# Kernel tuning notes

Hardware: AMD Instinct MI355X
Metric: run time of the kernel (lower is better)

Reference implementation:

```python
import jax, jax.numpy as jnp
import numpy as np

EPS = 1e-6
TAU = 0.07


def setup_inputs() -> dict:
    key = jax.random.key(0)
    kx, ky = jax.random.split(key)
    B, D = 4096, 1024
    x = jax.random.normal(kx, (B, D), dtype=jnp.float32)
    y = jax.random.normal(ky, (B, D), dtype=jnp.float32)
    return {"x": x, "y": y}


def reference(x, y):
    B = x.shape[0]
    # torch CosineSimilarity: dot / (max(||x||, eps) * max(||y||, eps))
    xn = x / jnp.maximum(jnp.linalg.norm(x, axis=-1, keepdims=True), EPS)
    yn = y / jnp.maximum(jnp.linalg.norm(y, axis=-1, keepdims=True), EPS)
    S = jnp.einsum('id,jd->ij', xn, yn)          # [B, B] cosine sims, S[i,j]=cos(x_i,y_j)
    E = jnp.exp(S / TAU)                          # bounded: |S|<=1 so exp <= e^{1/0.07}
    diag = jnp.diagonal(E)
    # original: sum_j (exp + eps) + eps  ->  sum_j exp + B*eps + eps
    extra = B * EPS + EPS
    row_denom = jnp.sum(E, axis=1) + extra        # x->y direction (loop 1)
    col_denom = jnp.sum(E, axis=0) + extra        # y->x direction (loop 2)
    coef = -1.0 / (2.0 * B)
    loss = coef * (jnp.sum(jnp.log(diag / row_denom)) + jnp.sum(jnp.log(diag / col_denom)))
    return loss
```

## Files before the change

### kernel.cpp

```cpp
#include <hip/hip_runtime.h>
#include <hip/hip_bf16.h>

#define NB 4096
#define DK 1024
#define EPSF 1e-6f
#define QSCALE 16.0f

typedef __attribute__((ext_vector_type(8))) int   i32x8_t;
typedef __attribute__((ext_vector_type(4))) int   i32x4_t;
typedef __attribute__((ext_vector_type(4))) float f32x4_t;


__global__ __launch_bounds__(256) void normalize_rows(
    const float* __restrict__ x, const float* __restrict__ y,
    unsigned char* __restrict__ xq, unsigned char* __restrict__ yq,
    float* __restrict__ sdiag, float* __restrict__ zerobuf)
{
    const int t = threadIdx.x;
    const int gid = blockIdx.x * 256 + t;
    if (gid < 2 * NB) zerobuf[gid] = 0.f;

    const int wave = t >> 6;
    const int lane = t & 63;
    const int row  = blockIdx.x * 4 + wave;

    const float4* xr = reinterpret_cast<const float4*>(x + (size_t)row * DK);
    const float4* yr = reinterpret_cast<const float4*>(y + (size_t)row * DK);

    float4 xv[4], yv[4];
    float ssx = 0.f, ssy = 0.f, sxy = 0.f;
    #pragma unroll
    for (int jj = 0; jj < 4; ++jj) {
        xv[jj] = xr[lane * 4 + jj];
        yv[jj] = yr[lane * 4 + jj];
        ssx += xv[jj].x*xv[jj].x + xv[jj].y*xv[jj].y + xv[jj].z*xv[jj].z + xv[jj].w*xv[jj].w;
        ssy += yv[jj].x*yv[jj].x + yv[jj].y*yv[jj].y + yv[jj].z*yv[jj].z + yv[jj].w*yv[jj].w;
        sxy += xv[jj].x*yv[jj].x + xv[jj].y*yv[jj].y + xv[jj].z*yv[jj].z + xv[jj].w*yv[jj].w;
    }
    #pragma unroll
    for (int off = 1; off < 64; off <<= 1) {
        ssx += __shfl_xor(ssx, off, 64);
        ssy += __shfl_xor(ssy, off, 64);
        sxy += __shfl_xor(sxy, off, 64);
    }
    const float invx = 1.0f / fmaxf(sqrtf(ssx), EPSF);
    const float invy = 1.0f / fmaxf(sqrtf(ssy), EPSF);
    const float sx = invx * QSCALE;
    const float sy = invy * QSCALE;

    i32x4_t xb, yb;
    #pragma unroll
    for (int jj = 0; jj < 4; ++jj) {
        int px = __builtin_amdgcn_cvt_pk_fp8_f32(xv[jj].x * sx, xv[jj].y * sx, 0, false);
        px     = __builtin_amdgcn_cvt_pk_fp8_f32(xv[jj].z * sx, xv[jj].w * sx, px, true);
        int py = __builtin_amdgcn_cvt_pk_fp8_f32(yv[jj].x * sy, yv[jj].y * sy, 0, false);
        py     = __builtin_amdgcn_cvt_pk_fp8_f32(yv[jj].z * sy, yv[jj].w * sy, py, true);
        xb[jj] = px;
        yb[jj] = py;
    }

    const int p = row >> 4, r = row & 15;
    const unsigned off = (unsigned)(p * 32 + (lane >> 3) * 4 + ((lane >> 1) & 3)) * 512
                       + r * 32 + (lane & 1) * 16;
    *reinterpret_cast<i32x4_t*>(xq + off) = xb;
    *reinterpret_cast<i32x4_t*>(yq + off) = yb;

    if (lane == 0) sdiag[row] = sxy * invx * invy;
}

__device__ __forceinline__ i32x8_t ldfrag(const unsigned char* p) {
    const i32x4_t lo = *reinterpret_cast<const i32x4_t*>(p);
    const i32x4_t hi = *reinterpret_cast<const i32x4_t*>(p + 16);
    i32x8_t r;
    r[0] = lo[0]; r[1] = lo[1]; r[2] = lo[2]; r[3] = lo[3];
    r[4] = hi[0]; r[5] = hi[1]; r[6] = hi[2]; r[7] = hi[3];
    return r;
}

__global__ __launch_bounds__(256) void gemm_exp_sums(
    const unsigned char* __restrict__ xq, const unsigned char* __restrict__ yq,
    float* __restrict__ rowsum, float* __restrict__ colsum)
{
    const int t    = threadIdx.x;
    const int lane = t & 63;
    const int wave = t >> 6;
    const int q    = lane >> 4;
    const int l15  = lane & 15;

    const int R0 = blockIdx.y * 128;
    const int C0 = blockIdx.x * 128;
    const int wRow = (wave >> 1) * 64;
    const int wCol = (wave & 1) * 64;

    f32x4_t acc[4][4];
    #pragma unroll
    for (int i = 0; i < 4; i++)
        #pragma unroll
        for (int j = 0; j < 4; j++)
            acc[i][j] = (f32x4_t){0.f, 0.f, 0.f, 0.f};

    const unsigned char* Abase =
        xq + (size_t)(((R0 + wRow) >> 4) * 32 + q) * 512 + l15 * 32;
    const unsigned char* Bbase =
        yq + (size_t)(((C0 + wCol) >> 4) * 32 + q) * 512 + l15 * 32;

    const int kb0 = (2 * wave + (blockIdx.x & 1)) & 7;

    #pragma unroll 1
    for (int s = 0; s < 8; ++s) {
        const int kb = (kb0 + s) & 7;
        const unsigned char* Ak = Abase + kb * 2048;
        const unsigned char* Bk = Bbase + kb * 2048;

        i32x8_t bfr[4], afr[4];
        #pragma unroll
        for (int nt = 0; nt < 4; ++nt) bfr[nt] = ldfrag(Bk + nt * 16384);
        #pragma unroll
        for (int mt = 0; mt < 4; ++mt) afr[mt] = ldfrag(Ak + mt * 16384);

        #pragma unroll
        for (int mt = 0; mt < 4; ++mt)
            #pragma unroll
            for (int nt = 0; nt < 4; ++nt)
                acc[mt][nt] = __builtin_amdgcn_mfma_scale_f32_16x16x128_f8f6f4(
                    afr[mt], bfr[nt], acc[mt][nt],
                    0, 0,
                    0, 0x7F7F7F7F,
                    0, 0x7F7F7F7F);
    }

    const float kScale = (float)(1.0 / (256.0 * 0.07 * 0.6931471805599453));
    float csum[4] = {0.f, 0.f, 0.f, 0.f};
    #pragma unroll
    for (int mt = 0; mt < 4; ++mt) {
        float rsum[4] = {0.f, 0.f, 0.f, 0.f};
        #pragma unroll
        for (int nt = 0; nt < 4; ++nt) {
            #pragma unroll
            for (int r = 0; r < 4; ++r) {
                const float e = exp2f(acc[mt][nt][r] * kScale);
                rsum[r]  += e;
                csum[nt] += e;
            }
        }
        #pragma unroll
        for (int r = 0; r < 4; ++r) {
            float v = rsum[r];
            v += __shfl_xor(v, 1, 64);
            v += __shfl_xor(v, 2, 64);
            v += __shfl_xor(v, 4, 64);
            v += __shfl_xor(v, 8, 64);
            if (l15 == 0)
                atomicAdd(&rowsum[R0 + wRow + mt * 16 + q * 4 + r], v);
        }
    }
    #pragma unroll
    for (int nt = 0; nt < 4; ++nt) {
        float v = csum[nt];
        v += __shfl_xor(v, 16, 64);
        v += __shfl_xor(v, 32, 64);
        if (lane < 16)
            atomicAdd(&colsum[C0 + wCol + nt * 16 + l15], v);
    }
}

__global__ __launch_bounds__(1024) void finalize(
    const float* __restrict__ rowsum, const float* __restrict__ colsum,
    const float* __restrict__ sdiag, float* __restrict__ out)
{
    const float extra = (float)(NB * 1e-6 + 1e-6);
    double local = 0.0;
    for (int i = threadIdx.x; i < NB; i += 1024) {
        local += (double)sdiag[i] * (2.0 / 0.07)
               - (double)logf(rowsum[i] + extra)
               - (double)logf(colsum[i] + extra);
    }
    #pragma unroll
    for (int off = 1; off < 64; off <<= 1)
        local += __shfl_xor(local, off, 64);
    __shared__ double dred[16];
    const int wave = threadIdx.x >> 6;
    if ((threadIdx.x & 63) == 0) dred[wave] = local;
    __syncthreads();
    if (threadIdx.x == 0) {
        double tot = 0.0;
        #pragma unroll
        for (int w = 0; w < 16; ++w) tot += dred[w];
        out[0] = (float)(tot * (-1.0 / (2.0 * NB)));
    }
}

extern "C" void kernel_launch(void* const* d_in, const int* in_sizes, int n_in,
                              void* d_out, int out_size, void* d_ws, size_t ws_size,
                              hipStream_t stream)
{
    const float* x = (const float*)d_in[0];
    const float* y = (const float*)d_in[1];
    float* out = (float*)d_out;

    char* ws = (char*)d_ws;
    unsigned char* xq = (unsigned char*)ws;
    unsigned char* yq = (unsigned char*)(ws + (size_t)4 * 1024 * 1024);
    float* rowsum = (float*)(ws + (size_t)8 * 1024 * 1024);
    float* colsum = rowsum + NB;
    float* sdiag  = colsum + NB;

    normalize_rows<<<NB / 4, 256, 0, stream>>>(x, y, xq, yq, sdiag, rowsum);

    dim3 grid(NB / 128, NB / 128);
    gemm_exp_sums<<<grid, 256, 0, stream>>>(xq, yq, rowsum, colsum);

    finalize<<<1, 1024, 0, stream>>>(rowsum, colsum, sdiag, out);
}
```

Measured before the change: 116.6 us.

## Stage FP8 tiles in LDS via async loads with 256x256 block tiles

The GEMM kernel now stages the A and B fp8 tiles in shared memory using global_load_lds async copies, instead of having every wave load its fragments straight from global memory. Block tiles grow to 256x256 with 512 threads, and each wave computes a 128x64 output across two row halves. The quantized layout written by normalize_rows changes to a 128-byte row stride with an XOR swizzle so the LDS fragment reads avoid bank conflicts. The aim is more operand reuse and less global traffic. The cost is 64KB of LDS per block, two barriers per k-step with no double buffering so loads do not overlap compute, and only 256 blocks in the grid.

```diff
diff --git a/kernel.cpp b/kernel.cpp
--- a/kernel.cpp
+++ b/kernel.cpp
@@ -10,6 +10,12 @@
 typedef __attribute__((ext_vector_type(4))) int   i32x4_t;
 typedef __attribute__((ext_vector_type(4))) float f32x4_t;
 
+
+__device__ __forceinline__ void async16(const void* g, void* lds) {
+    __builtin_amdgcn_global_load_lds(
+        (const __attribute__((address_space(1))) void*)g,
+        (__attribute__((address_space(3))) void*)lds, 16, 0, 0);
+}
 
 __global__ __launch_bounds__(256) void normalize_rows(
     const float* __restrict__ x, const float* __restrict__ y,
@@ -60,98 +66,118 @@
     }
 
     const int p = row >> 4, r = row & 15;
-    const unsigned off = (unsigned)(p * 32 + (lane >> 3) * 4 + ((lane >> 1) & 3)) * 512
-                       + r * 32 + (lane & 1) * 16;
+    const unsigned off = (unsigned)(p * 32 + (lane >> 3) * 4) * 512
+                       + r * 128 + ((((lane & 7) ^ (r & 7))) << 4);
     *reinterpret_cast<i32x4_t*>(xq + off) = xb;
     *reinterpret_cast<i32x4_t*>(yq + off) = yb;
 
     if (lane == 0) sdiag[row] = sxy * invx * invy;
 }
 
-__device__ __forceinline__ i32x8_t ldfrag(const unsigned char* p) {
-    const i32x4_t lo = *reinterpret_cast<const i32x4_t*>(p);
-    const i32x4_t hi = *reinterpret_cast<const i32x4_t*>(p + 16);
-    i32x8_t r;
-    r[0] = lo[0]; r[1] = lo[1]; r[2] = lo[2]; r[3] = lo[3];
-    r[4] = hi[0]; r[5] = hi[1]; r[6] = hi[2]; r[7] = hi[3];
-    return r;
-}
-
-__global__ __launch_bounds__(256) void gemm_exp_sums(
+__global__ __launch_bounds__(512) void gemm_exp_sums(
     const unsigned char* __restrict__ xq, const unsigned char* __restrict__ yq,
     float* __restrict__ rowsum, float* __restrict__ colsum)
 {
+    __shared__ __align__(16) unsigned char As[32 * 1024];
+    __shared__ __align__(16) unsigned char Bs[32 * 1024];
+
     const int t    = threadIdx.x;
     const int lane = t & 63;
     const int wave = t >> 6;
     const int q    = lane >> 4;
     const int l15  = lane & 15;
 
-    const int R0 = blockIdx.y * 128;
-    const int C0 = blockIdx.x * 128;
-    const int wRow = (wave >> 1) * 64;
-    const int wCol = (wave & 1) * 64;
-
-    f32x4_t acc[4][4];
-    #pragma unroll
-    for (int i = 0; i < 4; i++)
-        #pragma unroll
-        for (int j = 0; j < 4; j++)
-            acc[i][j] = (f32x4_t){0.f, 0.f, 0.f, 0.f};
-
-    const unsigned char* Abase =
-        xq + (size_t)(((R0 + wRow) >> 4) * 32 + q) * 512 + l15 * 32;
-    const unsigned char* Bbase =
-        yq + (size_t)(((C0 + wCol) >> 4) * 32 + q) * 512 + l15 * 32;
-
-    const int kb0 = (2 * wave + (blockIdx.x & 1)) & 7;
+    const int R0 = blockIdx.y * 256;
+    const int C0 = blockIdx.x * 256;
+    const int wRow = (wave >> 2) * 64;
+    const int wCol = (wave & 3) * 64;
+
+    f32x4_t acc[2][4][4];
+    #pragma unroll
+    for (int hh = 0; hh < 2; hh++)
+        #pragma unroll
+        for (int i = 0; i < 4; i++)
+            #pragma unroll
+            for (int j = 0; j < 4; j++)
+                acc[hh][i][j] = (f32x4_t){0.f, 0.f, 0.f, 0.f};
+
+    const unsigned char* srcA =
+        xq + (size_t)((R0 >> 4) + wave) * 16384 + lane * 16;
+    const unsigned char* srcB =
+        yq + (size_t)((C0 >> 4) + wave) * 16384 + lane * 16;
+
+    const int sLo = (((2 * q)    ) ^ (l15 & 7)) << 4;
+    const int sHi = (((2 * q) + 1) ^ (l15 & 7)) << 4;
 
     #pragma unroll 1
-    for (int s = 0; s < 8; ++s) {
-        const int kb = (kb0 + s) & 7;
-        const unsigned char* Ak = Abase + kb * 2048;
-        const unsigned char* Bk = Bbase + kb * 2048;
-
-        i32x8_t bfr[4], afr[4];
-        #pragma unroll
-        for (int nt = 0; nt < 4; ++nt) bfr[nt] = ldfrag(Bk + nt * 16384);
-        #pragma unroll
-        for (int mt = 0; mt < 4; ++mt) afr[mt] = ldfrag(Ak + mt * 16384);
-
-        #pragma unroll
-        for (int mt = 0; mt < 4; ++mt)
-            #pragma unroll
-            for (int nt = 0; nt < 4; ++nt)
-                acc[mt][nt] = __builtin_amdgcn_mfma_scale_f32_16x16x128_f8f6f4(
-                    afr[mt], bfr[nt], acc[mt][nt],
-                    0, 0,
-                    0, 0x7F7F7F7F,
-                    0, 0x7F7F7F7F);
+    for (int kb = 0; kb < 8; ++kb) {
+        __syncthreads();
+        #pragma unroll
+        for (int h2 = 0; h2 < 2; ++h2) {
+            async16(srcA + kb * 2048 + h2 * 1024,          &As[wave * 2048 + h2 * 1024]);
+            async16(srcA + kb * 2048 + h2 * 1024 + 131072, &As[(wave + 8) * 2048 + h2 * 1024]);
+            async16(srcB + kb * 2048 + h2 * 1024,          &Bs[wave * 2048 + h2 * 1024]);
+            async16(srcB + kb * 2048 + h2 * 1024 + 131072, &Bs[(wave + 8) * 2048 + h2 * 1024]);
+        }
+        __syncthreads();
+
+        i32x8_t bfr[4];
+        #pragma unroll
+        for (int nt = 0; nt < 4; ++nt) {
+            const unsigned char* c = &Bs[((wCol >> 4) + nt) * 2048 + l15 * 128];
+            const i32x4_t lo = *reinterpret_cast<const i32x4_t*>(c + sLo);
+            const i32x4_t hi = *reinterpret_cast<const i32x4_t*>(c + sHi);
+            bfr[nt][0] = lo[0]; bfr[nt][1] = lo[1]; bfr[nt][2] = lo[2]; bfr[nt][3] = lo[3];
+            bfr[nt][4] = hi[0]; bfr[nt][5] = hi[1]; bfr[nt][6] = hi[2]; bfr[nt][7] = hi[3];
+        }
+        #pragma unroll
+        for (int hh = 0; hh < 2; ++hh) {
+            #pragma unroll
+            for (int mt = 0; mt < 4; ++mt) {
+                const unsigned char* c =
+                    &As[((wRow >> 4) + hh * 8 + mt) * 2048 + l15 * 128];
+                const i32x4_t lo = *reinterpret_cast<const i32x4_t*>(c + sLo);
+                const i32x4_t hi = *reinterpret_cast<const i32x4_t*>(c + sHi);
+                i32x8_t af;
+                af[0] = lo[0]; af[1] = lo[1]; af[2] = lo[2]; af[3] = lo[3];
+                af[4] = hi[0]; af[5] = hi[1]; af[6] = hi[2]; af[7] = hi[3];
+                #pragma unroll
+                for (int nt = 0; nt < 4; ++nt)
+                    acc[hh][mt][nt] = __builtin_amdgcn_mfma_scale_f32_16x16x128_f8f6f4(
+                        af, bfr[nt], acc[hh][mt][nt],
+                        0, 0,
+                        0, 0x7F7F7F7F,
+                        0, 0x7F7F7F7F);
+            }
+        }
     }
 
     const float kScale = (float)(1.0 / (256.0 * 0.07 * 0.6931471805599453));
     float csum[4] = {0.f, 0.f, 0.f, 0.f};
     #pragma unroll
-    for (int mt = 0; mt < 4; ++mt) {
-        float rsum[4] = {0.f, 0.f, 0.f, 0.f};
-        #pragma unroll
-        for (int nt = 0; nt < 4; ++nt) {
+    for (int hh = 0; hh < 2; ++hh) {
+        #pragma unroll
+        for (int mt = 0; mt < 4; ++mt) {
+            float rsum[4] = {0.f, 0.f, 0.f, 0.f};
+            #pragma unroll
+            for (int nt = 0; nt < 4; ++nt) {
+                #pragma unroll
+                for (int r = 0; r < 4; ++r) {
+                    const float e = exp2f(acc[hh][mt][nt][r] * kScale);
+                    rsum[r]  += e;
+                    csum[nt] += e;
+                }
+            }
             #pragma unroll
             for (int r = 0; r < 4; ++r) {
-                const float e = exp2f(acc[mt][nt][r] * kScale);
-                rsum[r]  += e;
-                csum[nt] += e;
+                float v = rsum[r];
+                v += __shfl_xor(v, 1, 64);
+                v += __shfl_xor(v, 2, 64);
+                v += __shfl_xor(v, 4, 64);
+                v += __shfl_xor(v, 8, 64);
+                if (l15 == 0)
+                    atomicAdd(&rowsum[R0 + wRow + hh * 128 + mt * 16 + q * 4 + r], v);
             }
-        }
-        #pragma unroll
-        for (int r = 0; r < 4; ++r) {
-            float v = rsum[r];
-            v += __shfl_xor(v, 1, 64);
-            v += __shfl_xor(v, 2, 64);
-            v += __shfl_xor(v, 4, 64);
-            v += __shfl_xor(v, 8, 64);
-            if (l15 == 0)
-                atomicAdd(&rowsum[R0 + wRow + mt * 16 + q * 4 + r], v);
         }
     }
     #pragma unroll
@@ -207,8 +233,8 @@
 
     normalize_rows<<<NB / 4, 256, 0, stream>>>(x, y, xq, yq, sdiag, rowsum);
 
-    dim3 grid(NB / 128, NB / 128);
-    gemm_exp_sums<<<grid, 256, 0, stream>>>(xq, yq, rowsum, colsum);
+    dim3 grid(16, 16);
+    gemm_exp_sums<<<grid, 512, 0, stream>>>(xq, yq, rowsum, colsum);
 
     finalize<<<1, 1024, 0, stream>>>(rowsum, colsum, sdiag, out);
 }
```

After: 107.4 us. 7.9% less time.
